# Optimization experiments

Measured on AMD Instinct MI355X. Metric: run time of the kernel, lower is better.

Reference implementation:

```python
import jax, jax.numpy as jnp
import numpy as np

D_MODEL = 1024
HEADS = 16
DK = D_MODEL // HEADS
LAYERS = 4
BATCH = 8
SEQ = 1024
EPS = 1e-5


def _ln2(x):
    # torch LayerNorm([seq_len, d_model]) with default (untrained) affine: gamma=1, beta=0
    m = jnp.mean(x, axis=(1, 2), keepdims=True)
    v = jnp.var(x, axis=(1, 2), keepdims=True)
    return (x - m) * jax.lax.rsqrt(v + EPS)


def _pos_enc(seq_len, d_model):
    pos = jnp.arange(seq_len, dtype=jnp.float32)[:, None]
    i = jnp.arange(d_model)
    angle = pos / jnp.power(1000.0, (2 * (i // 2)).astype(jnp.float32) / d_model)
    return jnp.where(i % 2 == 0, jnp.sin(angle), jnp.cos(angle))  # [S, D]


def setup_inputs() -> dict:
    key = jax.random.key(0)
    ks = jax.random.split(key, 12)
    s = 0.02
    X = jax.random.normal(ks[0], (BATCH, SEQ, D_MODEL), dtype=jnp.float32)
    Wq = jax.random.normal(ks[1], (LAYERS, HEADS, DK, D_MODEL), dtype=jnp.float32) * s
    Wk = jax.random.normal(ks[2], (LAYERS, HEADS, DK, D_MODEL), dtype=jnp.float32) * s
    Wv = jax.random.normal(ks[3], (LAYERS, HEADS, DK, D_MODEL), dtype=jnp.float32) * s
    W0 = jax.random.normal(ks[4], (LAYERS, D_MODEL, D_MODEL), dtype=jnp.float32) * s
    Wr_w = jax.random.normal(ks[5], (LAYERS, D_MODEL, D_MODEL), dtype=jnp.float32) * s
    Wr_b = jax.random.normal(ks[6], (LAYERS, D_MODEL), dtype=jnp.float32) * s
    Wf0_w = jax.random.normal(ks[7], (LAYERS, D_MODEL, D_MODEL), dtype=jnp.float32) * s
    Wf0_b = jax.random.normal(ks[8], (LAYERS, D_MODEL), dtype=jnp.float32) * s
    Wf1_w = jax.random.normal(ks[9], (LAYERS, D_MODEL, D_MODEL), dtype=jnp.float32) * s
    Wf1_b = jax.random.normal(ks[10], (LAYERS, D_MODEL), dtype=jnp.float32) * s
    return {"X": X, "Wq": Wq, "Wk": Wk, "Wv": Wv, "W0": W0,
            "Wr_w": Wr_w, "Wr_b": Wr_b, "Wf0_w": Wf0_w, "Wf0_b": Wf0_b,
            "Wf1_w": Wf1_w, "Wf1_b": Wf1_b}


def reference(X, Wq, Wk, Wv, W0, Wr_w, Wr_b, Wf0_w, Wf0_b, Wf1_w, Wf1_b):
    B, S, D = X.shape
    x = X + _pos_enc(S, D)[None]
    scale = 1.0 / jnp.sqrt(jnp.float32(DK))
    for l in range(LAYERS):
        # batched multi-head projections (equivalent to per-head Linear + concat)
        Q = jnp.einsum('bsd,hkd->bhsk', x, Wq[l])
        K = jnp.einsum('bsd,hkd->bhsk', x, Wk[l])
        V = jnp.einsum('bsd,hkd->bhsk', x, Wv[l])
        scores = jnp.einsum('bhsk,bhtk->bhst', Q, K) * scale
        A = jax.nn.softmax(scores, axis=-1)
        O = jnp.einsum('bhst,bhtk->bhsk', A, V)
        O = O.transpose(0, 2, 1, 3).reshape(B, S, D)  # concat heads on feature dim
        mha = O @ W0[l].T
        r0 = _ln2(x + mha) @ Wr_w[l].T + Wr_b[l]
        ff = jax.nn.relu(r0 @ Wf0_w[l].T + Wf0_b[l]) @ Wf1_w[l].T + Wf1_b[l]
        x = _ln2(ff + r0) @ Wr_w[l].T + Wr_b[l]
    return x
```

## Files before the change

kernel.cpp:

```cpp
#include <hip/hip_runtime.h>
#include <hip/hip_bf16.h>
#include <math.h>

#define D_MODEL 1024
#define HEADS   16
#define DKV     64
#define LAYERS  4
#define BATCH   8
#define SEQ     1024
#define NTOK    (BATCH*SEQ)
#define LN_N    (SEQ*D_MODEL)
#define EPSV    1e-5f

typedef __attribute__((ext_vector_type(8))) short short8;
typedef __attribute__((ext_vector_type(4))) float floatx4;

__device__ __forceinline__ float bf2f(ushort u) {
    union { uint i; float f; } v; v.i = ((uint)u) << 16; return v.f;
}
__device__ __forceinline__ ushort f2bf(float f) {
    union { float f; uint i; } v; v.f = f;
    uint r = (v.i + 0x7fffu + ((v.i >> 16) & 1u)) >> 16;
    return (ushort)r;
}
__device__ __forceinline__ uint cvtpk(float a, float b) {
    uint r;
    asm("v_cvt_pk_bf16_f32 %0, %1, %2" : "=v"(r) : "v"(a), "v"(b));
    return r;
}

__device__ __forceinline__ void gload16(const ushort* g, ushort* l) {
    __builtin_amdgcn_global_load_lds(
        (const __attribute__((address_space(1))) void*)g,
        (__attribute__((address_space(3))) void*)l, 16, 0, 0);
}

#define TBUF (128*32)
__device__ __forceinline__ void gemm_core128(
    const ushort* __restrict__ A, const ushort* __restrict__ B,
    int lda, int ldb, int Kd,
    ushort* ldsA, ushort* ldsB, floatx4 (&acc)[4][4])
{
    const int tid  = threadIdx.x;
    const int lane = tid & 63;
    const int w    = tid >> 6;
    const int wm   = w >> 1, wn = w & 1;
    const int mn   = lane & 15, quad = lane >> 4;
    const int srow = tid >> 2;
    const int scol = (tid & 3) * 8;
    const ushort* ga = A + (size_t)srow * lda + scol;
    const ushort* gb = B + (size_t)srow * ldb + scol;
    ushort* la = ldsA + srow * 32 + scol;
    ushort* lb = ldsB + srow * 32 + scol;

    gload16(ga, la);
    gload16(ga + (size_t)64 * lda, la + 64 * 32);
    gload16(gb, lb);
    gload16(gb + (size_t)64 * ldb, lb + 64 * 32);
    __syncthreads();

    int cur = 0;
    for (int k0 = 0; k0 < Kd; k0 += 32) {
        const int nxt = cur ^ 1;
        if (k0 + 32 < Kd) {
            gload16(ga + k0 + 32, la + nxt * TBUF);
            gload16(ga + (size_t)64 * lda + k0 + 32, la + nxt * TBUF + 64 * 32);
            gload16(gb + k0 + 32, lb + nxt * TBUF);
            gload16(gb + (size_t)64 * ldb + k0 + 32, lb + nxt * TBUF + 64 * 32);
        }
        const ushort* cA = ldsA + cur * TBUF;
        const ushort* cB = ldsB + cur * TBUF;
        short8 af[4], bfr[4];
#pragma unroll
        for (int i = 0; i < 4; i++)
            af[i] = *(const short8*)(cA + (wm * 64 + i * 16 + mn) * 32 + quad * 8);
#pragma unroll
        for (int j = 0; j < 4; j++)
            bfr[j] = *(const short8*)(cB + (wn * 64 + j * 16 + mn) * 32 + quad * 8);
#pragma unroll
        for (int i = 0; i < 4; i++)
#pragma unroll
            for (int j = 0; j < 4; j++)
                acc[i][j] = __builtin_amdgcn_mfma_f32_16x16x32_bf16(af[i], bfr[j], acc[i][j], 0, 0, 0);
        __syncthreads();
        cur = nxt;
    }
}

__global__ __launch_bounds__(256) void gemm_bt128(
    const ushort* __restrict__ A, const ushort* __restrict__ B,
    const float* __restrict__ bias, ushort* __restrict__ C,
    const ushort* __restrict__ resid, float* __restrict__ stats,
    float* __restrict__ outF, int relu)
{
    __shared__ ushort ldsA[2 * TBUF], ldsB[2 * TBUF];
    __shared__ float sred1[4], sred2[4];
    const int lid = blockIdx.y * 64 + blockIdx.x;
    const int xcd = lid & 7, idx = lid >> 3;
    const int bx = xcd * 8 + (idx >> 3);
    const int by = idx & 7;
    floatx4 acc[4][4];
#pragma unroll
    for (int i = 0; i < 4; i++)
#pragma unroll
        for (int j = 0; j < 4; j++) acc[i][j] = (floatx4){0.f, 0.f, 0.f, 0.f};

    gemm_core128(A + (size_t)bx * 128 * D_MODEL,
                 B + (size_t)by * 128 * D_MODEL,
                 D_MODEL, D_MODEL, D_MODEL, ldsA, ldsB, acc);

    const int lane = threadIdx.x & 63, w = threadIdx.x >> 6;
    const int wm = w >> 1, wn = w & 1;
    const int mn = lane & 15, quad = lane >> 4;
    float ssum = 0.f, ssq = 0.f;
#pragma unroll
    for (int i = 0; i < 4; i++) {
#pragma unroll
        for (int j = 0; j < 4; j++) {
            int col = by * 128 + wn * 64 + j * 16 + mn;
            float bv = bias ? bias[col] : 0.f;
#pragma unroll
            for (int r = 0; r < 4; r++) {
                int row = bx * 128 + wm * 64 + i * 16 + quad * 4 + r;
                float v = acc[i][j][r] + bv;
                if (relu) v = fmaxf(v, 0.f);
                if (resid) {
                    v += bf2f(resid[(size_t)row * D_MODEL + col]);
                    ssum += v; ssq += v * v;
                }
                if (outF) outF[(size_t)row * D_MODEL + col] = v;
                else      C[(size_t)row * D_MODEL + col] = f2bf(v);
            }
        }
    }
    if (stats) {
        for (int o = 1; o < 64; o <<= 1) {
            ssum += __shfl_xor(ssum, o); ssq += __shfl_xor(ssq, o);
        }
        if (lane == 0) { sred1[w] = ssum; sred2[w] = ssq; }
        __syncthreads();
        if (threadIdx.x == 0) {
            int b = bx >> 3;
            atomicAdd(&stats[b * 32],      sred1[0] + sred1[1] + sred1[2] + sred1[3]);
            atomicAdd(&stats[b * 32 + 16], sred2[0] + sred2[1] + sred2[2] + sred2[3]);
        }
    }
}

__global__ __launch_bounds__(256) void gemm_qkv(
    const ushort* __restrict__ X, const ushort* __restrict__ Wq,
    const ushort* __restrict__ Wk, const ushort* __restrict__ Wv,
    ushort* __restrict__ Q, ushort* __restrict__ K, ushort* __restrict__ Vt)
{
    __shared__ ushort ldsA[2 * TBUF], ldsB[2 * TBUF];
    const int lid = blockIdx.y * 64 + blockIdx.x;
    const int xcd = lid & 7, idx = lid >> 3;
    const int bx = xcd * 8 + idx / 24;
    const int byy = idx % 24;
    const int which = byy >> 3;
    const int nb = byy & 7;
    const ushort* B = (which == 0) ? Wq : (which == 1) ? Wk : Wv;
    floatx4 acc[4][4];
#pragma unroll
    for (int i = 0; i < 4; i++)
#pragma unroll
        for (int j = 0; j < 4; j++) acc[i][j] = (floatx4){0.f, 0.f, 0.f, 0.f};

    gemm_core128(X + (size_t)bx * 128 * D_MODEL,
                 B + (size_t)nb * 128 * D_MODEL,
                 D_MODEL, D_MODEL, D_MODEL, ldsA, ldsB, acc);

    const int lane = threadIdx.x & 63, w = threadIdx.x >> 6;
    const int wm = w >> 1, wn = w & 1;
    const int mn = lane & 15, quad = lane >> 4;
    if (which == 2) {
#pragma unroll
        for (int i = 0; i < 4; i++) {
#pragma unroll
            for (int j = 0; j < 4; j++) {
                int col = nb * 128 + wn * 64 + j * 16 + mn;
                int h = col >> 6, kk = col & 63;
                int row0 = bx * 128 + wm * 64 + i * 16 + quad * 4;
                int b = row0 >> 10, t0 = row0 & 1023;
                uint2 uu;
                uu.x = cvtpk(acc[i][j][0], acc[i][j][1]);
                uu.y = cvtpk(acc[i][j][2], acc[i][j][3]);
                *(uint2*)(Vt + (((size_t)(b * HEADS + h)) * DKV + kk) * SEQ + t0) = uu;
            }
        }
    } else {
        ushort* dst = (which == 0) ? Q : K;
#pragma unroll
        for (int i = 0; i < 4; i++) {
#pragma unroll
            for (int j = 0; j < 4; j++) {
                int col = nb * 128 + wn * 64 + j * 16 + mn;
#pragma unroll
                for (int r = 0; r < 4; r++) {
                    int row = bx * 128 + wm * 64 + i * 16 + quad * 4 + r;
                    dst[(size_t)row * D_MODEL + col] = f2bf(acc[i][j][r]);
                }
            }
        }
    }
}

#define SQK 72
#define SV  136
__global__ __launch_bounds__(256) void flash_attn(
    const ushort* __restrict__ Q, const ushort* __restrict__ K,
    const ushort* __restrict__ Vt, ushort* __restrict__ O)
{
    __shared__ ushort lQ[128 * SQK];
    __shared__ ushort lK[128 * SQK];
    __shared__ ushort lV[64 * SV];
    const int tid = threadIdx.x, lane = tid & 63, w = tid >> 6;
    const int mn = lane & 15, quad = lane >> 4;
    const int pair = blockIdx.x;
    const int qt = blockIdx.y;
    const int b = pair >> 4, h = pair & 15;
    const ushort* Qb = Q + ((size_t)b * SEQ) * D_MODEL + h * DKV;
    const ushort* Kb = K + ((size_t)b * SEQ) * D_MODEL + h * DKV;
    const ushort* Vb = Vt + (size_t)pair * DKV * SEQ;

#pragma unroll
    for (int c = 0; c < 4; c++) {
        int idx = c * 256 + tid;
        int row = idx >> 3, col = (idx & 7) * 8;
        short8 qv = *(const short8*)(Qb + (size_t)(qt * 128 + row) * D_MODEL + col);
        short8 qs;
#pragma unroll
        for (int e = 0; e < 8; e++) qs[e] = (short)f2bf(bf2f((ushort)qv[e]) * 0.125f);
        *(short8*)(lQ + row * SQK + col) = qs;
    }
    short8 kreg[4], vreg[4];
#pragma unroll
    for (int c = 0; c < 4; c++) {
        int idx = c * 256 + tid;
        int row = idx >> 3, col = (idx & 7) * 8;
        kreg[c] = *(const short8*)(Kb + (size_t)row * D_MODEL + col);
        int vr = idx >> 4, vc = (idx & 15) * 8;
        vreg[c] = *(const short8*)(Vb + (size_t)vr * SEQ + vc);
    }
    __syncthreads();

    short8 bq[2][2];
#pragma unroll
    for (int i = 0; i < 2; i++)
#pragma unroll
        for (int kk = 0; kk < 2; kk++)
            bq[i][kk] = *(const short8*)(lQ + (w * 32 + i * 16 + mn) * SQK + kk * 32 + quad * 8);

#pragma unroll
    for (int c = 0; c < 4; c++) {
        int idx = c * 256 + tid;
        int row = idx >> 3, col = (idx & 7) * 8;
        *(short8*)(lK + row * SQK + col) = kreg[c];
        int vr = idx >> 4, vc = (idx & 15) * 8;
        *(short8*)(lV + vr * SV + vc) = vreg[c];
    }
    __syncthreads();

    floatx4 acc_o[2][4];
    float lrow[2] = {0.f, 0.f};
#pragma unroll
    for (int i = 0; i < 2; i++)
#pragma unroll
        for (int jo = 0; jo < 4; jo++) acc_o[i][jo] = (floatx4){0.f, 0.f, 0.f, 0.f};

    for (int tk = 0; tk < 8; tk++) {
        if (tk < 7) {
#pragma unroll
            for (int c = 0; c < 4; c++) {
                int idx = c * 256 + tid;
                int row = idx >> 3, col = (idx & 7) * 8;
                kreg[c] = *(const short8*)(Kb + (size_t)((tk + 1) * 128 + row) * D_MODEL + col);
                int vr = idx >> 4, vc = (idx & 15) * 8;
                vreg[c] = *(const short8*)(Vb + (size_t)vr * SEQ + (tk + 1) * 128 + vc);
            }
        }

        floatx4 s[2][8];
#pragma unroll
        for (int i = 0; i < 2; i++)
#pragma unroll
            for (int j = 0; j < 8; j++) s[i][j] = (floatx4){0.f, 0.f, 0.f, 0.f};
        __builtin_amdgcn_s_setprio(1);
#pragma unroll
        for (int kk = 0; kk < 2; kk++) {
#pragma unroll
            for (int j = 0; j < 8; j++) {
                short8 ak = *(const short8*)(lK + (j * 16 + mn) * SQK + kk * 32 + quad * 8);
                s[0][j] = __builtin_amdgcn_mfma_f32_16x16x32_bf16(ak, bq[0][kk], s[0][j], 0, 0, 0);
                s[1][j] = __builtin_amdgcn_mfma_f32_16x16x32_bf16(ak, bq[1][kk], s[1][j], 0, 0, 0);
            }
        }
        __builtin_amdgcn_s_setprio(0);

#pragma unroll
        for (int i = 0; i < 2; i++) {
            float ps = 0.f;
#pragma unroll
            for (int j = 0; j < 8; j++)
#pragma unroll
                for (int r = 0; r < 4; r++) {
                    float p = __expf(s[i][j][r]);
                    s[i][j][r] = p;
                    ps += p;
                }
            ps += __shfl_xor(ps, 16);
            ps += __shfl_xor(ps, 32);
            lrow[i] += ps;
        }

#pragma unroll
        for (int hf = 0; hf < 2; hf++) {
#pragma unroll
            for (int i = 0; i < 2; i++)
#pragma unroll
                for (int jl = 0; jl < 4; jl++) {
                    int j = hf * 4 + jl;
                    uint2 uu;
                    uu.x = cvtpk(s[i][j][0], s[i][j][1]);
                    uu.y = cvtpk(s[i][j][2], s[i][j][3]);
                    *(uint2*)(lQ + (w * 32 + i * 16 + mn) * SQK + jl * 16 + quad * 4) = uu;
                }
            __builtin_amdgcn_s_setprio(1);
#pragma unroll
            for (int kkl = 0; kkl < 2; kkl++) {
                int kk = hf * 2 + kkl;
                short8 pa0 = *(const short8*)(lQ + (w * 32 + 0  + mn) * SQK + kkl * 32 + quad * 8);
                short8 pa1 = *(const short8*)(lQ + (w * 32 + 16 + mn) * SQK + kkl * 32 + quad * 8);
#pragma unroll
                for (int jo = 0; jo < 4; jo++) {
                    short8 bv = *(const short8*)(lV + (jo * 16 + mn) * SV + kk * 32 + quad * 8);
                    acc_o[0][jo] = __builtin_amdgcn_mfma_f32_16x16x32_bf16(pa0, bv, acc_o[0][jo], 0, 0, 0);
                    acc_o[1][jo] = __builtin_amdgcn_mfma_f32_16x16x32_bf16(pa1, bv, acc_o[1][jo], 0, 0, 0);
                }
            }
            __builtin_amdgcn_s_setprio(0);
        }

        __syncthreads();
        if (tk < 7) {
#pragma unroll
            for (int c = 0; c < 4; c++) {
                int idx = c * 256 + tid;
                int row = idx >> 3, col = (idx & 7) * 8;
                *(short8*)(lK + row * SQK + col) = kreg[c];
                int vr = idx >> 4, vc = (idx & 15) * 8;
                *(short8*)(lV + vr * SV + vc) = vreg[c];
            }
            __syncthreads();
        }
    }

#pragma unroll
    for (int i = 0; i < 2; i++)
#pragma unroll
        for (int r = 0; r < 4; r++) {
            float rs = __shfl(lrow[i], quad * 4 + r);
            float rinv = 1.f / rs;
            int row = qt * 128 + w * 32 + i * 16 + quad * 4 + r;
#pragma unroll
            for (int jo = 0; jo < 4; jo++)
                O[((size_t)b * SEQ + row) * D_MODEL + h * DKV + jo * 16 + mn] =
                    f2bf(acc_o[i][jo][r] * rinv);
        }
}

__global__ __launch_bounds__(256) void cvt_f32_bf16(const float* __restrict__ src,
                                                    ushort* __restrict__ dst) {
    size_t base = ((size_t)blockIdx.x * 256 + threadIdx.x) * 8;
    float4 a = *(const float4*)(src + base);
    float4 b = *(const float4*)(src + base + 4);
    short8 o;
    o[0] = (short)f2bf(a.x); o[1] = (short)f2bf(a.y);
    o[2] = (short)f2bf(a.z); o[3] = (short)f2bf(a.w);
    o[4] = (short)f2bf(b.x); o[5] = (short)f2bf(b.y);
    o[6] = (short)f2bf(b.z); o[7] = (short)f2bf(b.w);
    *(short8*)(dst + base) = o;
}

__global__ __launch_bounds__(256) void add_pos(const float* __restrict__ X,
                                               ushort* __restrict__ x) {
    size_t idx = (size_t)blockIdx.x * 256 + threadIdx.x;
    int d = (int)(idx & (D_MODEL - 1));
    int s = (int)((idx >> 10) & (SEQ - 1));
    float freq = powf(1000.f, (float)(2 * (d >> 1)) * (1.f / (float)D_MODEL));
    float ang = (float)s / freq;
    float pe = (d & 1) ? cosf(ang) : sinf(ang);
    x[idx] = f2bf(X[idx] + pe);
}

__global__ __launch_bounds__(256) void ln_apply(
    const ushort* __restrict__ S, ushort* __restrict__ Y,
    const float* __restrict__ stats)
{
    size_t base = ((size_t)blockIdx.x * 256 + threadIdx.x) * 8;
    int b = blockIdx.x >> 9;
    float mean = stats[b * 32] * (1.f / (float)LN_N);
    float var = stats[b * 32 + 16] * (1.f / (float)LN_N) - mean * mean;
    float r = rsqrtf(var + EPSV);
    short8 sv = *(const short8*)(S + base);
    short8 ov;
#pragma unroll
    for (int i = 0; i < 8; i++) ov[i] = (short)f2bf((bf2f((ushort)sv[i]) - mean) * r);
    *(short8*)(Y + base) = ov;
}

__global__ void zero_stats(float* stats) { stats[threadIdx.x] = 0.f; }

extern "C" void kernel_launch(void* const* d_in, const int* in_sizes, int n_in,
                              void* d_out, int out_size, void* d_ws, size_t ws_size,
                              hipStream_t stream) {
    const float* X    = (const float*)d_in[0];
    const float* Wq   = (const float*)d_in[1];
    const float* Wk   = (const float*)d_in[2];
    const float* Wv   = (const float*)d_in[3];
    const float* W0   = (const float*)d_in[4];
    const float* Wr_w = (const float*)d_in[5];
    const float* Wr_b = (const float*)d_in[6];
    const float* Wf0w = (const float*)d_in[7];
    const float* Wf0b = (const float*)d_in[8];
    const float* Wf1w = (const float*)d_in[9];
    const float* Wf1b = (const float*)d_in[10];
    float* out = (float*)d_out;

    char* ws = (char*)d_ws;
    size_t off = 0;
    auto alloc = [&](size_t bytes) -> void* {
        void* p = ws + off; off += (bytes + 255) & ~(size_t)255; return p;
    };
    const size_t ACT = (size_t)NTOK * D_MODEL * sizeof(ushort);
    const size_t WTE = (size_t)LAYERS * D_MODEL * D_MODEL;
    ushort* x  = (ushort*)alloc(ACT);
    ushort* bQ = (ushort*)alloc(ACT);
    ushort* bK = (ushort*)alloc(ACT);
    ushort* bV = (ushort*)alloc(ACT);
    ushort* bO = (ushort*)alloc(ACT);
    ushort* wq  = (ushort*)alloc(WTE * 2);
    ushort* wk  = (ushort*)alloc(WTE * 2);
    ushort* wv  = (ushort*)alloc(WTE * 2);
    ushort* w0  = (ushort*)alloc(WTE * 2);
    ushort* wr  = (ushort*)alloc(WTE * 2);
    ushort* wf0 = (ushort*)alloc(WTE * 2);
    ushort* wf1 = (ushort*)alloc(WTE * 2);
    float* stats = (float*)alloc(256 * sizeof(float));

    const int EW_BLOCKS = (NTOK * D_MODEL) / (256 * 8);
    const int CVT_BLOCKS = (int)(WTE / (256 * 8));
    const dim3 GEMM_GRID(NTOK / 128, D_MODEL / 128);
    const dim3 QKV_GRID(NTOK / 128, 3 * D_MODEL / 128);
    const dim3 FLASH_GRID(BATCH * HEADS, SEQ / 128);

    cvt_f32_bf16<<<CVT_BLOCKS, 256, 0, stream>>>(Wq,   wq);
    cvt_f32_bf16<<<CVT_BLOCKS, 256, 0, stream>>>(Wk,   wk);
    cvt_f32_bf16<<<CVT_BLOCKS, 256, 0, stream>>>(Wv,   wv);
    cvt_f32_bf16<<<CVT_BLOCKS, 256, 0, stream>>>(W0,   w0);
    cvt_f32_bf16<<<CVT_BLOCKS, 256, 0, stream>>>(Wr_w, wr);
    cvt_f32_bf16<<<CVT_BLOCKS, 256, 0, stream>>>(Wf0w, wf0);
    cvt_f32_bf16<<<CVT_BLOCKS, 256, 0, stream>>>(Wf1w, wf1);

    add_pos<<<(NTOK * D_MODEL) / 256, 256, 0, stream>>>(X, x);

    for (int l = 0; l < LAYERS; l++) {
        const size_t WO = (size_t)l * D_MODEL * D_MODEL;
        const ushort* Wq_l  = wq  + WO;
        const ushort* Wk_l  = wk  + WO;
        const ushort* Wv_l  = wv  + WO;
        const ushort* W0_l  = w0  + WO;
        const ushort* Wr_l  = wr  + WO;
        const ushort* W0w_l = wf0 + WO;
        const ushort* W1w_l = wf1 + WO;
        const float* Wrb_l = Wr_b + (size_t)l * D_MODEL;
        const float* W0b_l = Wf0b + (size_t)l * D_MODEL;
        const float* W1b_l = Wf1b + (size_t)l * D_MODEL;

        gemm_qkv<<<QKV_GRID, 256, 0, stream>>>(x, Wq_l, Wk_l, Wv_l, bQ, bK, bV);

        flash_attn<<<FLASH_GRID, 256, 0, stream>>>(bQ, bK, bV, bO);

        zero_stats<<<1, 256, 0, stream>>>(stats);
        gemm_bt128<<<GEMM_GRID, 256, 0, stream>>>(bO, W0_l, nullptr, bK,
            x, stats, nullptr, 0);
        ln_apply<<<EW_BLOCKS, 256, 0, stream>>>(bK, bO, stats);
        gemm_bt128<<<GEMM_GRID, 256, 0, stream>>>(bO, Wr_l, Wrb_l, bV,
            nullptr, nullptr, nullptr, 0);
        gemm_bt128<<<GEMM_GRID, 256, 0, stream>>>(bV, W0w_l, W0b_l, bQ,
            nullptr, nullptr, nullptr, 1);
        zero_stats<<<1, 256, 0, stream>>>(stats);
        gemm_bt128<<<GEMM_GRID, 256, 0, stream>>>(bQ, W1w_l, W1b_l, bK,
            bV, stats, nullptr, 0);
        ln_apply<<<EW_BLOCKS, 256, 0, stream>>>(bK, bO, stats);
        gemm_bt128<<<GEMM_GRID, 256, 0, stream>>>(bO, Wr_l, Wrb_l, x,
            nullptr, nullptr, (l == LAYERS - 1) ? out : nullptr, 0);
    }
}
```

Baseline: 1.629 ms.

## Rework flash attention with direct-to-LDS swizzled loads and register-resident P

Folds the 1/sqrt(dk) scale into the Q projection epilogue, so Q fragments load straight from global memory without LDS staging. K and V tiles are loaded with global_load_lds into XOR-swizzled unpadded LDS buffers, and the next tile's load is issued right after the buffer's last use. The softmax probabilities stay in registers and are rearranged into MFMA A-operand layout with permlane swap instructions, replacing the LDS round-trip. This cuts LDS traffic and register-staged copies but relies on correct swizzle and permlane lane mappings, and it loses the double-buffered overlap between compute and the next load.

```diff
diff --git a/kernel.cpp b/kernel.cpp
--- a/kernel.cpp
+++ b/kernel.cpp
@@ -27,6 +27,12 @@
     uint r;
     asm("v_cvt_pk_bf16_f32 %0, %1, %2" : "=v"(r) : "v"(a), "v"(b));
     return r;
+}
+__device__ __forceinline__ void pl32(uint &a, uint &c) {
+    asm volatile("v_permlane32_swap_b32 %0, %1" : "+v"(a), "+v"(c));
+}
+__device__ __forceinline__ void pl16(uint &a, uint &c) {
+    asm volatile("v_permlane16_swap_b32 %0, %1" : "+v"(a), "+v"(c));
 }
 
 __device__ __forceinline__ void gload16(const ushort* g, ushort* l) {
@@ -190,6 +196,7 @@
         }
     } else {
         ushort* dst = (which == 0) ? Q : K;
+        const float scl = (which == 0) ? 0.125f : 1.0f;
 #pragma unroll
         for (int i = 0; i < 4; i++) {
 #pragma unroll
@@ -198,22 +205,19 @@
 #pragma unroll
                 for (int r = 0; r < 4; r++) {
                     int row = bx * 128 + wm * 64 + i * 16 + quad * 4 + r;
-                    dst[(size_t)row * D_MODEL + col] = f2bf(acc[i][j][r]);
+                    dst[(size_t)row * D_MODEL + col] = f2bf(acc[i][j][r] * scl);
                 }
             }
         }
     }
 }
 
-#define SQK 72
-#define SV  136
 __global__ __launch_bounds__(256) void flash_attn(
     const ushort* __restrict__ Q, const ushort* __restrict__ K,
     const ushort* __restrict__ Vt, ushort* __restrict__ O)
 {
-    __shared__ ushort lQ[128 * SQK];
-    __shared__ ushort lK[128 * SQK];
-    __shared__ ushort lV[64 * SV];
+    __shared__ ushort lK[64 * 128];
+    __shared__ ushort lV[64 * 128];
     const int tid = threadIdx.x, lane = tid & 63, w = tid >> 6;
     const int mn = lane & 15, quad = lane >> 4;
     const int pair = blockIdx.x;
@@ -223,42 +227,37 @@
     const ushort* Kb = K + ((size_t)b * SEQ) * D_MODEL + h * DKV;
     const ushort* Vb = Vt + (size_t)pair * DKV * SEQ;
 
-#pragma unroll
-    for (int c = 0; c < 4; c++) {
-        int idx = c * 256 + tid;
-        int row = idx >> 3, col = (idx & 7) * 8;
-        short8 qv = *(const short8*)(Qb + (size_t)(qt * 128 + row) * D_MODEL + col);
-        short8 qs;
-#pragma unroll
-        for (int e = 0; e < 8; e++) qs[e] = (short)f2bf(bf2f((ushort)qv[e]) * 0.125f);
-        *(short8*)(lQ + row * SQK + col) = qs;
-    }
-    short8 kreg[4], vreg[4];
-#pragma unroll
-    for (int c = 0; c < 4; c++) {
-        int idx = c * 256 + tid;
-        int row = idx >> 3, col = (idx & 7) * 8;
-        kreg[c] = *(const short8*)(Kb + (size_t)row * D_MODEL + col);
-        int vr = idx >> 4, vc = (idx & 15) * 8;
-        vreg[c] = *(const short8*)(Vb + (size_t)vr * SEQ + vc);
-    }
-    __syncthreads();
-
     short8 bq[2][2];
 #pragma unroll
     for (int i = 0; i < 2; i++)
 #pragma unroll
         for (int kk = 0; kk < 2; kk++)
-            bq[i][kk] = *(const short8*)(lQ + (w * 32 + i * 16 + mn) * SQK + kk * 32 + quad * 8);
-
-#pragma unroll
-    for (int c = 0; c < 4; c++) {
-        int idx = c * 256 + tid;
-        int row = idx >> 3, col = (idx & 7) * 8;
-        *(short8*)(lK + row * SQK + col) = kreg[c];
-        int vr = idx >> 4, vc = (idx & 15) * 8;
-        *(short8*)(lV + vr * SV + vc) = vreg[c];
-    }
+            bq[i][kk] = *(const short8*)(Qb +
+                (size_t)(qt * 128 + w * 32 + i * 16 + mn) * D_MODEL + kk * 32 + quad * 8);
+
+    auto stage_K = [&](int tkk) {
+#pragma unroll
+        for (int c = 0; c < 4; c++) {
+            int lin = c * 256 + tid;
+            int rw = lin >> 4;
+            int cc0 = (lin & 15) ^ (rw & 7);
+            int r = rw + ((cc0 >> 3) << 6);
+            gload16(Kb + (size_t)(tkk * 128 + r) * D_MODEL + (cc0 & 7) * 8,
+                    lK + lin * 8);
+        }
+    };
+    auto stage_V = [&](int tkk) {
+#pragma unroll
+        for (int c = 0; c < 4; c++) {
+            int lin = c * 256 + tid;
+            int rw = lin >> 4;
+            int cc0 = (lin & 15) ^ (rw & 7);
+            gload16(Vb + (size_t)rw * SEQ + tkk * 128 + cc0 * 8,
+                    lV + lin * 8);
+        }
+    };
+
+    stage_K(0); stage_V(0);
     __syncthreads();
 
     floatx4 acc_o[2][4];
@@ -269,17 +268,6 @@
         for (int jo = 0; jo < 4; jo++) acc_o[i][jo] = (floatx4){0.f, 0.f, 0.f, 0.f};
 
     for (int tk = 0; tk < 8; tk++) {
-        if (tk < 7) {
-#pragma unroll
-            for (int c = 0; c < 4; c++) {
-                int idx = c * 256 + tid;
-                int row = idx >> 3, col = (idx & 7) * 8;
-                kreg[c] = *(const short8*)(Kb + (size_t)((tk + 1) * 128 + row) * D_MODEL + col);
-                int vr = idx >> 4, vc = (idx & 15) * 8;
-                vreg[c] = *(const short8*)(Vb + (size_t)vr * SEQ + (tk + 1) * 128 + vc);
-            }
-        }
-
         floatx4 s[2][8];
 #pragma unroll
         for (int i = 0; i < 2; i++)
@@ -290,69 +278,57 @@
         for (int kk = 0; kk < 2; kk++) {
 #pragma unroll
             for (int j = 0; j < 8; j++) {
-                short8 ak = *(const short8*)(lK + (j * 16 + mn) * SQK + kk * 32 + quad * 8);
+                int krow = (j & 3) * 16 + mn;
+                int kch = (((j >> 2) * 8 + kk * 4 + quad) ^ (mn & 7));
+                short8 ak = *(const short8*)(lK + krow * 128 + kch * 8);
                 s[0][j] = __builtin_amdgcn_mfma_f32_16x16x32_bf16(ak, bq[0][kk], s[0][j], 0, 0, 0);
                 s[1][j] = __builtin_amdgcn_mfma_f32_16x16x32_bf16(ak, bq[1][kk], s[1][j], 0, 0, 0);
             }
         }
         __builtin_amdgcn_s_setprio(0);
-
+        __syncthreads();
+        if (tk < 7) stage_K(tk + 1);
+
+        uint pw[2][8][2];
 #pragma unroll
         for (int i = 0; i < 2; i++) {
             float ps = 0.f;
 #pragma unroll
-            for (int j = 0; j < 8; j++)
-#pragma unroll
-                for (int r = 0; r < 4; r++) {
-                    float p = __expf(s[i][j][r]);
-                    s[i][j][r] = p;
-                    ps += p;
-                }
+            for (int j = 0; j < 8; j++) {
+                float p0 = __expf(s[i][j][0]), p1 = __expf(s[i][j][1]);
+                float p2 = __expf(s[i][j][2]), p3 = __expf(s[i][j][3]);
+                ps += (p0 + p1) + (p2 + p3);
+                pw[i][j][0] = cvtpk(p0, p1);
+                pw[i][j][1] = cvtpk(p2, p3);
+            }
             ps += __shfl_xor(ps, 16);
             ps += __shfl_xor(ps, 32);
             lrow[i] += ps;
         }
 
-#pragma unroll
-        for (int hf = 0; hf < 2; hf++) {
-#pragma unroll
-            for (int i = 0; i < 2; i++)
-#pragma unroll
-                for (int jl = 0; jl < 4; jl++) {
-                    int j = hf * 4 + jl;
-                    uint2 uu;
-                    uu.x = cvtpk(s[i][j][0], s[i][j][1]);
-                    uu.y = cvtpk(s[i][j][2], s[i][j][3]);
-                    *(uint2*)(lQ + (w * 32 + i * 16 + mn) * SQK + jl * 16 + quad * 4) = uu;
-                }
-            __builtin_amdgcn_s_setprio(1);
-#pragma unroll
-            for (int kkl = 0; kkl < 2; kkl++) {
-                int kk = hf * 2 + kkl;
-                short8 pa0 = *(const short8*)(lQ + (w * 32 + 0  + mn) * SQK + kkl * 32 + quad * 8);
-                short8 pa1 = *(const short8*)(lQ + (w * 32 + 16 + mn) * SQK + kkl * 32 + quad * 8);
-#pragma unroll
-                for (int jo = 0; jo < 4; jo++) {
-                    short8 bv = *(const short8*)(lV + (jo * 16 + mn) * SV + kk * 32 + quad * 8);
-                    acc_o[0][jo] = __builtin_amdgcn_mfma_f32_16x16x32_bf16(pa0, bv, acc_o[0][jo], 0, 0, 0);
-                    acc_o[1][jo] = __builtin_amdgcn_mfma_f32_16x16x32_bf16(pa1, bv, acc_o[1][jo], 0, 0, 0);
-                }
-            }
-            __builtin_amdgcn_s_setprio(0);
-        }
-
+        __builtin_amdgcn_s_setprio(1);
+#pragma unroll
+        for (int kk = 0; kk < 4; kk++) {
+            union { short8 s8; uint u[4]; } pa[2];
+#pragma unroll
+            for (int i = 0; i < 2; i++) {
+                uint A = pw[i][2 * kk][0],     Bw = pw[i][2 * kk][1];
+                uint C = pw[i][2 * kk + 1][0], D  = pw[i][2 * kk + 1][1];
+                pl32(A, C);  pl16(A, C);
+                pl32(Bw, D); pl16(Bw, D);
+                pa[i].u[0] = A; pa[i].u[1] = Bw; pa[i].u[2] = C; pa[i].u[3] = D;
+            }
+#pragma unroll
+            for (int jo = 0; jo < 4; jo++) {
+                int vch = ((kk * 4 + quad) ^ (mn & 7));
+                short8 bv = *(const short8*)(lV + (jo * 16 + mn) * 128 + vch * 8);
+                acc_o[0][jo] = __builtin_amdgcn_mfma_f32_16x16x32_bf16(pa[0].s8, bv, acc_o[0][jo], 0, 0, 0);
+                acc_o[1][jo] = __builtin_amdgcn_mfma_f32_16x16x32_bf16(pa[1].s8, bv, acc_o[1][jo], 0, 0, 0);
+            }
+        }
+        __builtin_amdgcn_s_setprio(0);
         __syncthreads();
-        if (tk < 7) {
-#pragma unroll
-            for (int c = 0; c < 4; c++) {
-                int idx = c * 256 + tid;
-                int row = idx >> 3, col = (idx & 7) * 8;
-                *(short8*)(lK + row * SQK + col) = kreg[c];
-                int vr = idx >> 4, vc = (idx & 15) * 8;
-                *(short8*)(lV + vr * SV + vc) = vreg[c];
-            }
-            __syncthreads();
-        }
+        if (tk < 7) stage_V(tk + 1);
     }
 
 #pragma unroll
```

Result: faster. 1.501 ms (-7.9%).
